# Optimization experiments

Measured on AMD Instinct MI355X. Metric: run time of the kernel, lower is better.

## Reference

```python
import jax, jax.numpy as jnp
import numpy as np

N_BOX = 20  # hardcoded boxes-per-frame in the original module


def setup_inputs() -> dict:
    key = jax.random.key(0)
    T = 256
    # boxes in [0,1); inter_area is clamped at 0 so degenerate boxes are fine,
    # and the (+1) terms in the areas keep denominators positive.
    rois = jax.random.uniform(key, (T, N_BOX, 4), dtype=jnp.float32)
    return {"rois": rois}


def reference(rois):
    # rois: [T, 20, 4] with (x1, y1, x2, y2)
    T = rois.shape[0]
    a = rois[:-1, :, None, :]  # frame t   boxes -> [T-1, 20, 1, 4]
    b = rois[1:, None, :, :]   # frame t+1 boxes -> [T-1, 1, 20, 4]

    ix1 = jnp.maximum(a[..., 0], b[..., 0])
    ix2 = jnp.minimum(a[..., 2], b[..., 2])
    iy1 = jnp.maximum(a[..., 1], b[..., 1])
    iy2 = jnp.minimum(a[..., 3], b[..., 3])
    inter = jnp.maximum(ix2 - ix1, 0.0) * jnp.maximum(iy2 - iy1, 0.0)

    area_a = (a[..., 2] - a[..., 0] + 1.0) * (a[..., 3] - a[..., 1] + 1.0)
    # faithful to source bug: second factor uses b[2]-b[1], not b[3]-b[1]
    area_b = (b[..., 2] - b[..., 0] + 1.0) * (b[..., 2] - b[..., 1] + 1.0)

    iou = inter / (area_a + area_b - inter)  # [T-1, 20, 20]

    # original writes block t at offset 20*(t-1); t=0 wraps (negative index)
    dest = (jnp.arange(T - 1) - 1) % T
    blocks = jnp.zeros((T, N_BOX, N_BOX), dtype=rois.dtype).at[dest].set(iou)

    r = jnp.arange(T)
    adj = jnp.zeros((T, N_BOX, T, N_BOX), dtype=rois.dtype)
    adj = adj.at[r, :, r, :].set(blocks)  # block-diagonal placement
    return adj.reshape(1, T * N_BOX, T * N_BOX)
```

## Files before the change

### kernel.cpp

```cpp
#include <hip/hip_runtime.h>


#define TT 256
#define NB 20
#define DIM (TT * NB)
#define DIM4 (DIM / 4)
#define RPB 4

__global__ void __launch_bounds__(256) fused_iou_diag_kernel(
        const float4* __restrict__ rois, float4* __restrict__ out) {
    const int wave = threadIdx.x >> 6;
    const int lane = threadIdx.x & 63;
    const int row  = blockIdx.x * RPB + wave;
    const int kr   = row / NB;
    const int ri   = row - kr * NB;

    const bool active = (kr != 254);
    const int t  = (kr == 255) ? 0 : kr + 1;
    const int tb = active ? t + 1 : 0;

    const float4 a = rois[t * NB + ri];
    const float area_a = (a.z - a.x + 1.f) * (a.w - a.y + 1.f);

    const int bcol0 = kr * (NB / 4);
    const float4* brow = rois + tb * NB;
    float4* rowp = out + (size_t)row * DIM4;

    #pragma unroll
    for (int k = 0; k < DIM4 / 64; ++k) {
        const int c4 = (k << 6) + lane;
        float4 v = make_float4(0.f, 0.f, 0.f, 0.f);
        const int j4 = c4 - bcol0;
        if (active && (unsigned)j4 < (unsigned)(NB / 4)) {
            float* vp = (float*)&v;
            #pragma unroll
            for (int q = 0; q < 4; ++q) {
                const float4 b = brow[j4 * 4 + q];
                const float ix1 = fmaxf(a.x, b.x);
                const float ix2 = fminf(a.z, b.z);
                const float iy1 = fmaxf(a.y, b.y);
                const float iy2 = fminf(a.w, b.w);
                const float inter =
                    fmaxf(ix2 - ix1, 0.f) * fmaxf(iy2 - iy1, 0.f);
                const float area_b = (b.z - b.x + 1.f) * (b.z - b.y + 1.f);
                vp[q] = inter / (area_a + area_b - inter);
            }
        }
        rowp[c4] = v;
    }
}

extern "C" void kernel_launch(void* const* d_in, const int* in_sizes, int n_in,
                              void* d_out, int out_size, void* d_ws, size_t ws_size,
                              hipStream_t stream) {
    const float4* rois = (const float4*)d_in[0];
    float4* out = (float4*)d_out;
    fused_iou_diag_kernel<<<DIM / RPB, 256, 0, stream>>>(rois, out);
}
```

Measured before the change: 107.1 us.

## Zero output with hipMemsetAsync and compute only diagonal IoU blocks

Dense zero-filling of the 5120x5120 output now goes to a runtime memset instead of the compute kernel, and the kernel shrinks to 255 small blocks that write only the 20x20 diagonal IoU blocks. The aim is to let the runtime's fill path handle the large zero write and to drop the per-element branch from the hot store loop. It adds a second stream operation and its launch overhead, and the output is written twice for the diagonal elements.

```diff
diff --git a/kernel.cpp b/kernel.cpp
--- a/kernel.cpp
+++ b/kernel.cpp
@@ -5,49 +5,38 @@
 #define NB 20
 #define DIM (TT * NB)
 #define DIM4 (DIM / 4)
-#define RPB 4
 
-__global__ void __launch_bounds__(256) fused_iou_diag_kernel(
+__global__ void __launch_bounds__(128) diag_iou_kernel(
         const float4* __restrict__ rois, float4* __restrict__ out) {
-    const int wave = threadIdx.x >> 6;
-    const int lane = threadIdx.x & 63;
-    const int row  = blockIdx.x * RPB + wave;
-    const int kr   = row / NB;
-    const int ri   = row - kr * NB;
+    const int bid = blockIdx.x;
+    const int kr  = (bid == 254) ? 255 : bid;
+    const int t   = (kr == 255) ? 0 : kr + 1;
 
-    const bool active = (kr != 254);
-    const int t  = (kr == 255) ? 0 : kr + 1;
-    const int tb = active ? t + 1 : 0;
+    const int tid = threadIdx.x;
+    if (tid >= 100) return;
+    const int ri = tid / 5;
+    const int j4 = tid % 5;
 
     const float4 a = rois[t * NB + ri];
     const float area_a = (a.z - a.x + 1.f) * (a.w - a.y + 1.f);
+    const float4* brow = rois + (t + 1) * NB;
 
-    const int bcol0 = kr * (NB / 4);
-    const float4* brow = rois + tb * NB;
-    float4* rowp = out + (size_t)row * DIM4;
+    float4 v;
+    float* vp = (float*)&v;
+    #pragma unroll
+    for (int q = 0; q < 4; ++q) {
+        const float4 b = brow[j4 * 4 + q];
+        const float ix1 = fmaxf(a.x, b.x);
+        const float ix2 = fminf(a.z, b.z);
+        const float iy1 = fmaxf(a.y, b.y);
+        const float iy2 = fminf(a.w, b.w);
+        const float inter = fmaxf(ix2 - ix1, 0.f) * fmaxf(iy2 - iy1, 0.f);
+        const float area_b = (b.z - b.x + 1.f) * (b.z - b.y + 1.f);
+        vp[q] = inter / (area_a + area_b - inter);
+    }
 
-    #pragma unroll
-    for (int k = 0; k < DIM4 / 64; ++k) {
-        const int c4 = (k << 6) + lane;
-        float4 v = make_float4(0.f, 0.f, 0.f, 0.f);
-        const int j4 = c4 - bcol0;
-        if (active && (unsigned)j4 < (unsigned)(NB / 4)) {
-            float* vp = (float*)&v;
-            #pragma unroll
-            for (int q = 0; q < 4; ++q) {
-                const float4 b = brow[j4 * 4 + q];
-                const float ix1 = fmaxf(a.x, b.x);
-                const float ix2 = fminf(a.z, b.z);
-                const float iy1 = fmaxf(a.y, b.y);
-                const float iy2 = fminf(a.w, b.w);
-                const float inter =
-                    fmaxf(ix2 - ix1, 0.f) * fmaxf(iy2 - iy1, 0.f);
-                const float area_b = (b.z - b.x + 1.f) * (b.z - b.y + 1.f);
-                vp[q] = inter / (area_a + area_b - inter);
-            }
-        }
-        rowp[c4] = v;
-    }
+    const int row = kr * NB + ri;
+    out[(size_t)row * DIM4 + kr * 5 + j4] = v;
 }
 
 extern "C" void kernel_launch(void* const* d_in, const int* in_sizes, int n_in,
@@ -55,5 +44,6 @@
                               hipStream_t stream) {
     const float4* rois = (const float4*)d_in[0];
     float4* out = (float4*)d_out;
-    fused_iou_diag_kernel<<<DIM / RPB, 256, 0, stream>>>(rois, out);
+    hipMemsetAsync(d_out, 0, (size_t)DIM * DIM * sizeof(float), stream);
+    diag_iou_kernel<<<255, 128, 0, stream>>>(rois, out);
 }
```

After: 108.2 us. Within noise of the previous version (+1.0%).
